# Kernel tuning notes

Measured on AMD Instinct MI355X. Metric: run time of the kernel, lower is better.

The kernel has to match this reference:

```python
import jax, jax.numpy as jnp
import numpy as np
import math

B, NH, SQ, HD = 4, 32, 512, 128
MLEN = 3584


def setup_inputs() -> dict:
    key = jax.random.key(0)
    k1, k2, k3, k4 = jax.random.split(key, 4)
    q = jax.random.normal(k1, (B, NH, SQ, HD), dtype=jnp.float32)
    k = jax.random.normal(k2, (B, NH, SQ, HD), dtype=jnp.float32)
    v = jax.random.normal(k3, (B, NH, SQ, HD), dtype=jnp.float32)
    mem = jax.random.normal(k4, (B, MLEN, 2 * NH * HD), dtype=jnp.float32)
    mask = jnp.ones((B, 1, SQ, MLEN + SQ), dtype=jnp.float32)
    return {"q": q, "k": k, "v": v, "mask": mask, "mem": mem}


def reference(q, k, v, mask, mem):
    b, nh, sq, hd = k.shape
    mlen = mem.shape[1]
    # cache_kv: stack (k,v) -> (2,b,nh,sq,hd), permute -> (b,sq,2,nh,hd), flatten
    cache_kv = jnp.stack((k, v)).transpose(1, 3, 0, 2, 4).reshape(b, sq, 2 * nh * hd)
    # split cached mem into memk/memv: (b,mlen,2,nh,hd) -> (2,b,nh,mlen,hd)
    mem_r = mem.reshape(b, mlen, 2, nh, hd).transpose(2, 0, 3, 1, 4)
    k_full = jnp.concatenate([mem_r[0], k], axis=2)  # [b,nh,mlen+sq,hd]
    v_full = jnp.concatenate([mem_r[1], v], axis=2)
    scale = 1.0 / math.sqrt(hd)
    scores = jnp.einsum("bhqd,bhkd->bhqk", q * scale, k_full)
    # standard_attention general mask path (mask.shape[-2] != 1)
    scores = scores * mask - 10000.0 * (1.0 - mask)
    probs = jax.nn.softmax(scores, axis=-1)
    context = jnp.einsum("bhqk,bhkd->bhqd", probs, v_full)
    return context, cache_kv
```

## Files before the change

kernel.cpp:

```cpp
#include <hip/hip_runtime.h>

#define B_ 4
#define NH_ 32
#define SQ_ 512
#define HD_ 128
#define MLEN_ 3584
#define KT_ 4096
#define QB_ 128
#define KB_ 64
#define NTILE_ 64
#define MEMTILES_ 56

typedef float f32x4 __attribute__((ext_vector_type(4)));
typedef short s16x8 __attribute__((ext_vector_type(8)));

__device__ __forceinline__ f32x4 MFMA16(s16x8 a, s16x8 b, f32x4 c) {
    return __builtin_amdgcn_mfma_f32_16x16x32_bf16(a, b, c, 0, 0, 0);
}

__device__ __forceinline__ s16x8 cvt8(float4 a, float4 b) {
    union { s16x8 v; __bf16 h[8]; } u;
    u.h[0] = (__bf16)a.x; u.h[1] = (__bf16)a.y;
    u.h[2] = (__bf16)a.z; u.h[3] = (__bf16)a.w;
    u.h[4] = (__bf16)b.x; u.h[5] = (__bf16)b.y;
    u.h[6] = (__bf16)b.z; u.h[7] = (__bf16)b.w;
    return u.v;
}

__launch_bounds__(512, 4)
__global__ void attn_kernel(const float* __restrict__ q, const float* __restrict__ k,
                            const float* __restrict__ v, const float* __restrict__ mask,
                            const float* __restrict__ mem, float* __restrict__ ctx)
{
    __shared__ __bf16 Klds[KB_ * HD_];
    __shared__ __bf16 Vt[HD_ * KB_];

    const int tid  = threadIdx.x;
    const int lane = tid & 63;
    const int w    = tid >> 6;
    const int l15  = lane & 15;
    const int l4   = lane >> 4;
    const int xv   = (lane & 7) << 4;

    const int qt   = blockIdx.x >> 7;
    const int pair = blockIdx.x & 127;
    const int b    = pair >> 5;
    const int h    = pair & 31;
    const int q0   = qt * QB_;

    const float scale = 0.088388347648318447f;
    s16x8 qf[4];
    {
        const float* qbase = q + (((size_t)(b * NH_ + h)) * SQ_ + q0 + w * 16 + l15) * HD_;
        #pragma unroll
        for (int kc = 0; kc < 4; ++kc) {
            const float* p = qbase + kc * 32 + l4 * 8;
            float4 a = *(const float4*)p;
            float4 c = *(const float4*)(p + 4);
            a.x *= scale; a.y *= scale; a.z *= scale; a.w *= scale;
            c.x *= scale; c.y *= scale; c.z *= scale; c.w *= scale;
            qf[kc] = cvt8(a, c);
        }
    }

    f32x4 acc[8];
    #pragma unroll
    for (int n = 0; n < 8; ++n) acc[n] = (f32x4){0.f, 0.f, 0.f, 0.f};

    float mrun = -3.0e38f, lrun = 0.f;

    const float* maskrow = mask + ((size_t)b * SQ_ + q0 + w * 16 + l15) * KT_;

    for (int t = 0; t < NTILE_; ++t) {
        const int kv0 = t * KB_;
        const float *srcK, *srcV;
        int rstride;
        if (t < MEMTILES_) {
            const float* mrow = mem + ((size_t)b * MLEN_ + kv0) * (2 * NH_ * HD_) + h * HD_;
            srcK = mrow;
            srcV = mrow + NH_ * HD_;
            rstride = 2 * NH_ * HD_;
        } else {
            size_t off = (((size_t)b * NH_ + h) * SQ_ + (kv0 - MLEN_)) * HD_;
            srcK = k + off;
            srcV = v + off;
            rstride = HD_;
        }

        __syncthreads();

        #pragma unroll
        for (int it = 0; it < 2; ++it) {
            int idx = tid + it * 512;
            int row = idx >> 4, cg = idx & 15;
            const float* p = srcK + (size_t)row * rstride + cg * 8;
            float4 a = *(const float4*)p;
            float4 c = *(const float4*)(p + 4);
            s16x8 vv = cvt8(a, c);
            int byte = row * 256 + ((cg * 16) ^ ((row & 7) << 4));
            *(s16x8*)((char*)Klds + byte) = vv;
        }
        #pragma unroll
        for (int it = 0; it < 2; ++it) {
            int idx = tid + it * 512;
            int hd = idx & 127, kvb = idx >> 7;
            const float* p = srcV + (size_t)(kvb * 8) * rstride + hd;
            union { s16x8 v; __bf16 hh[8]; } u;
            #pragma unroll
            for (int j = 0; j < 8; ++j) u.hh[j] = (__bf16)p[(size_t)j * rstride];
            int byte = hd * 128 + ((kvb * 16) ^ ((hd & 7) << 4));
            *(s16x8*)((char*)Vt + byte) = u.v;
        }

        __syncthreads();

        f32x4 mk[4];
        #pragma unroll
        for (int mt = 0; mt < 4; ++mt)
            mk[mt] = *(const f32x4*)(maskrow + kv0 + mt * 16 + l4 * 4);

        f32x4 st[4];
        #pragma unroll
        for (int mt = 0; mt < 4; ++mt) st[mt] = (f32x4){0.f, 0.f, 0.f, 0.f};
        #pragma unroll
        for (int mt = 0; mt < 4; ++mt) {
            #pragma unroll
            for (int kc = 0; kc < 4; ++kc) {
                s16x8 kf = *(const s16x8*)((const char*)Klds +
                            (mt * 16 + l15) * 256 + (((kc * 4 + l4) * 16) ^ xv));
                st[mt] = MFMA16(kf, qf[kc], st[mt]);
            }
        }

        #pragma unroll
        for (int mt = 0; mt < 4; ++mt)
            #pragma unroll
            for (int r = 0; r < 4; ++r)
                st[mt][r] = fmaf(mk[mt][r], st[mt][r] + 10000.f, -10000.f);

        float x0 = fmaxf(fmaxf(st[0][0], st[0][1]), fmaxf(st[0][2], st[0][3]));
        float x1 = fmaxf(fmaxf(st[1][0], st[1][1]), fmaxf(st[1][2], st[1][3]));
        float x2 = fmaxf(fmaxf(st[2][0], st[2][1]), fmaxf(st[2][2], st[2][3]));
        float x3 = fmaxf(fmaxf(st[3][0], st[3][1]), fmaxf(st[3][2], st[3][3]));
        float rm = fmaxf(fmaxf(x0, x1), fmaxf(x2, x3));
        rm = fmaxf(rm, __shfl_xor(rm, 16));
        rm = fmaxf(rm, __shfl_xor(rm, 32));

        if (!__all(rm <= mrun + 8.f)) {
            float nm = fmaxf(mrun, rm);
            float al = __expf(mrun - nm);
            mrun = nm;
            lrun *= al;
            float alr0 = __shfl(al, l4 * 4 + 0);
            float alr1 = __shfl(al, l4 * 4 + 1);
            float alr2 = __shfl(al, l4 * 4 + 2);
            float alr3 = __shfl(al, l4 * 4 + 3);
            #pragma unroll
            for (int nn = 0; nn < 8; ++nn) {
                acc[nn][0] *= alr0; acc[nn][1] *= alr1;
                acc[nn][2] *= alr2; acc[nn][3] *= alr3;
            }
        }

        float rs = 0.f;
        #pragma unroll
        for (int mt = 0; mt < 4; ++mt) {
            #pragma unroll
            for (int r = 0; r < 4; ++r) {
                float pe = __expf(st[mt][r] - mrun);
                st[mt][r] = pe;
                rs += pe;
            }
        }
        rs += __shfl_xor(rs, 16);
        rs += __shfl_xor(rs, 32);
        lrun += rs;

        union PK { int d[2]; __bf16 hh[4]; };
        PK pk0, pk1, pk2, pk3;
        pk0.hh[0]=(__bf16)st[0][0]; pk0.hh[1]=(__bf16)st[0][1]; pk0.hh[2]=(__bf16)st[0][2]; pk0.hh[3]=(__bf16)st[0][3];
        pk1.hh[0]=(__bf16)st[1][0]; pk1.hh[1]=(__bf16)st[1][1]; pk1.hh[2]=(__bf16)st[1][2]; pk1.hh[3]=(__bf16)st[1][3];
        pk2.hh[0]=(__bf16)st[2][0]; pk2.hh[1]=(__bf16)st[2][1]; pk2.hh[2]=(__bf16)st[2][2]; pk2.hh[3]=(__bf16)st[2][3];
        pk3.hh[0]=(__bf16)st[3][0]; pk3.hh[1]=(__bf16)st[3][1]; pk3.hh[2]=(__bf16)st[3][2]; pk3.hh[3]=(__bf16)st[3][3];

        const int srcA = (l4 & 1) * 32 + l15;
        const int srcB = srcA + 16;
        const int sel  = l4 >> 1;
        s16x8 pa[2];
        {
            union { int d[4]; s16x8 v; } ua;
            int a00 = __shfl(pk0.d[0], srcA), a10 = __shfl(pk1.d[0], srcA);
            int a01 = __shfl(pk0.d[1], srcA), a11 = __shfl(pk1.d[1], srcA);
            int b00 = __shfl(pk0.d[0], srcB), b10 = __shfl(pk1.d[0], srcB);
            int b01 = __shfl(pk0.d[1], srcB), b11 = __shfl(pk1.d[1], srcB);
            ua.d[0] = sel ? a10 : a00; ua.d[1] = sel ? a11 : a01;
            ua.d[2] = sel ? b10 : b00; ua.d[3] = sel ? b11 : b01;
            pa[0] = ua.v;
        }
        {
            union { int d[4]; s16x8 v; } ua;
            int a00 = __shfl(pk2.d[0], srcA), a10 = __shfl(pk3.d[0], srcA);
            int a01 = __shfl(pk2.d[1], srcA), a11 = __shfl(pk3.d[1], srcA);
            int b00 = __shfl(pk2.d[0], srcB), b10 = __shfl(pk3.d[0], srcB);
            int b01 = __shfl(pk2.d[1], srcB), b11 = __shfl(pk3.d[1], srcB);
            ua.d[0] = sel ? a10 : a00; ua.d[1] = sel ? a11 : a01;
            ua.d[2] = sel ? b10 : b00; ua.d[3] = sel ? b11 : b01;
            pa[1] = ua.v;
        }

        #pragma unroll
        for (int nn = 0; nn < 8; ++nn) {
            s16x8 vf0 = *(const s16x8*)((const char*)Vt +
                          (nn * 16 + l15) * 128 + ((l4 * 16) ^ xv));
            s16x8 vf1 = *(const s16x8*)((const char*)Vt +
                          (nn * 16 + l15) * 128 + ((64 + l4 * 16) ^ xv));
            acc[nn] = MFMA16(pa[0], vf0, acc[nn]);
            acc[nn] = MFMA16(pa[1], vf1, acc[nn]);
        }
    }

    float lr0 = __shfl(lrun, l4 * 4 + 0);
    float lr1 = __shfl(lrun, l4 * 4 + 1);
    float lr2 = __shfl(lrun, l4 * 4 + 2);
    float lr3 = __shfl(lrun, l4 * 4 + 3);
    float inv0 = 1.f / lr0, inv1 = 1.f / lr1, inv2 = 1.f / lr2, inv3 = 1.f / lr3;
    float* obase = ctx + (((size_t)(b * NH_ + h)) * SQ_ + q0 + w * 16 + l4 * 4) * HD_ + l15;
    #pragma unroll
    for (int nn = 0; nn < 8; ++nn) {
        obase[(size_t)0 * HD_ + nn * 16] = acc[nn][0] * inv0;
        obase[(size_t)1 * HD_ + nn * 16] = acc[nn][1] * inv1;
        obase[(size_t)2 * HD_ + nn * 16] = acc[nn][2] * inv2;
        obase[(size_t)3 * HD_ + nn * 16] = acc[nn][3] * inv3;
    }
}

__global__ void cachekv_kernel(const float* __restrict__ k, const float* __restrict__ v,
                               float* __restrict__ out)
{
    size_t i = ((size_t)blockIdx.x * 256 + threadIdx.x) * 4;
    unsigned f = (unsigned)i;
    unsigned d    = f & 127;
    unsigned hh   = (f >> 7) & 31;
    unsigned part = (f >> 12) & 1;
    unsigned s    = (f >> 13) & 511;
    unsigned bb   = f >> 22;
    const float* src = (part ? v : k) + (((size_t)(bb * 32u + hh)) * 512u + s) * 128u + d;
    *(float4*)(out + i) = *(const float4*)src;
}

extern "C" void kernel_launch(void* const* d_in, const int* in_sizes, int n_in,
                              void* d_out, int out_size, void* d_ws, size_t ws_size,
                              hipStream_t stream) {
    const float* q    = (const float*)d_in[0];
    const float* k    = (const float*)d_in[1];
    const float* v    = (const float*)d_in[2];
    const float* mask = (const float*)d_in[3];
    const float* mem  = (const float*)d_in[4];
    float* out = (float*)d_out;

    attn_kernel<<<dim3(B_ * NH_ * (SQ_ / QB_)), dim3(512), 0, stream>>>(q, k, v, mask, mem, out);

    const int ctx_elems = B_ * NH_ * SQ_ * HD_;
    const int ckv_elems = B_ * SQ_ * 2 * NH_ * HD_;
    cachekv_kernel<<<dim3(ckv_elems / 4 / 256), dim3(256), 0, stream>>>(k, v, out + ctx_elems);
    (void)in_sizes; (void)n_in; (void)out_size; (void)d_ws; (void)ws_size;
}
```

Baseline: 322.1 us.

## Split attention KV range in two blocks and merge partials with reduce kernel

Splits the 64 KV tiles into two halves handled by separate blocks, doubling the grid from 512 to 1024 blocks. Each block writes its unnormalized partial output plus its running max and sum, and a new reduce kernel merges the two halves with log-sum-exp rescaling. The partial outputs are staged in the cache_kv output region before that region is overwritten, and max/sum pairs go to the workspace. The aim is better occupancy across the CUs. The cost is an extra write and read of the partial outputs, one more kernel launch, and the Q load and setup being repeated per half.

```diff
diff --git a/kernel.cpp b/kernel.cpp
--- a/kernel.cpp
+++ b/kernel.cpp
@@ -10,6 +10,7 @@
 #define KB_ 64
 #define NTILE_ 64
 #define MEMTILES_ 56
+#define HTILES_ 32
 
 typedef float f32x4 __attribute__((ext_vector_type(4)));
 typedef short s16x8 __attribute__((ext_vector_type(8)));
@@ -27,10 +28,11 @@
     return u.v;
 }
 
-__launch_bounds__(512, 4)
-__global__ void attn_kernel(const float* __restrict__ q, const float* __restrict__ k,
-                            const float* __restrict__ v, const float* __restrict__ mask,
-                            const float* __restrict__ mem, float* __restrict__ ctx)
+__launch_bounds__(512)
+__global__ void attn_split_kernel(const float* __restrict__ q, const float* __restrict__ k,
+                                  const float* __restrict__ v, const float* __restrict__ mask,
+                                  const float* __restrict__ mem,
+                                  float* __restrict__ opart, float2* __restrict__ ml)
 {
     __shared__ __bf16 Klds[KB_ * HD_];
     __shared__ __bf16 Vt[HD_ * KB_];
@@ -42,11 +44,13 @@
     const int l4   = lane >> 4;
     const int xv   = (lane & 7) << 4;
 
-    const int qt   = blockIdx.x >> 7;
+    const int half = blockIdx.x >> 9;
+    const int qt   = (blockIdx.x >> 7) & 3;
     const int pair = blockIdx.x & 127;
     const int b    = pair >> 5;
     const int h    = pair & 31;
     const int q0   = qt * QB_;
+    const int t0   = half * HTILES_;
 
     const float scale = 0.088388347648318447f;
     s16x8 qf[4];
@@ -71,7 +75,7 @@
 
     const float* maskrow = mask + ((size_t)b * SQ_ + q0 + w * 16 + l15) * KT_;
 
-    for (int t = 0; t < NTILE_; ++t) {
+    for (int t = t0; t < t0 + HTILES_; ++t) {
         const int kv0 = t * KB_;
         const float *srcK, *srcV;
         int rstride;
@@ -219,19 +223,41 @@
         }
     }
 
-    float lr0 = __shfl(lrun, l4 * 4 + 0);
-    float lr1 = __shfl(lrun, l4 * 4 + 1);
-    float lr2 = __shfl(lrun, l4 * 4 + 2);
-    float lr3 = __shfl(lrun, l4 * 4 + 3);
-    float inv0 = 1.f / lr0, inv1 = 1.f / lr1, inv2 = 1.f / lr2, inv3 = 1.f / lr3;
-    float* obase = ctx + (((size_t)(b * NH_ + h)) * SQ_ + q0 + w * 16 + l4 * 4) * HD_ + l15;
+    float* obase = opart + (size_t)half * (B_ * NH_ * SQ_ * HD_) +
+                   (((size_t)(b * NH_ + h)) * SQ_ + q0 + w * 16 + l4 * 4) * HD_ + l15;
     #pragma unroll
     for (int nn = 0; nn < 8; ++nn) {
-        obase[(size_t)0 * HD_ + nn * 16] = acc[nn][0] * inv0;
-        obase[(size_t)1 * HD_ + nn * 16] = acc[nn][1] * inv1;
-        obase[(size_t)2 * HD_ + nn * 16] = acc[nn][2] * inv2;
-        obase[(size_t)3 * HD_ + nn * 16] = acc[nn][3] * inv3;
+        obase[(size_t)0 * HD_ + nn * 16] = acc[nn][0];
+        obase[(size_t)1 * HD_ + nn * 16] = acc[nn][1];
+        obase[(size_t)2 * HD_ + nn * 16] = acc[nn][2];
+        obase[(size_t)3 * HD_ + nn * 16] = acc[nn][3];
     }
+    if (l4 == 0) {
+        int row = (b * NH_ + h) * SQ_ + q0 + w * 16 + l15;
+        ml[half * (B_ * NH_ * SQ_) + row] = make_float2(mrun, lrun);
+    }
+}
+
+__global__ void reduce_kernel(const float* __restrict__ part, const float2* __restrict__ ml,
+                              float* __restrict__ ctx)
+{
+    int idx = blockIdx.x * 256 + threadIdx.x;
+    int row = idx >> 5;
+    int c4  = (idx & 31) * 4;
+    float2 a = ml[row];
+    float2 c = ml[(B_ * NH_ * SQ_) + row];
+    float mm = fmaxf(a.x, c.x);
+    float e0 = __expf(a.x - mm), e1 = __expf(c.x - mm);
+    float inv = 1.f / (a.y * e0 + c.y * e1);
+    const float4 o0 = *(const float4*)(part + (size_t)row * HD_ + c4);
+    const float4 o1 = *(const float4*)(part + (size_t)(B_ * NH_ * SQ_) * HD_ +
+                                       (size_t)row * HD_ + c4);
+    float4 o;
+    o.x = (o0.x * e0 + o1.x * e1) * inv;
+    o.y = (o0.y * e0 + o1.y * e1) * inv;
+    o.z = (o0.z * e0 + o1.z * e1) * inv;
+    o.w = (o0.w * e0 + o1.w * e1) * inv;
+    *(float4*)(ctx + (size_t)row * HD_ + c4) = o;
 }
 
 __global__ void cachekv_kernel(const float* __restrict__ k, const float* __restrict__ v,
@@ -258,10 +284,18 @@
     const float* mem  = (const float*)d_in[4];
     float* out = (float*)d_out;
 
-    attn_kernel<<<dim3(B_ * NH_ * (SQ_ / QB_)), dim3(512), 0, stream>>>(q, k, v, mask, mem, out);
-
     const int ctx_elems = B_ * NH_ * SQ_ * HD_;
     const int ckv_elems = B_ * SQ_ * 2 * NH_ * HD_;
+
+    float*  part = out + ctx_elems;
+    float2* ml   = (float2*)d_ws;
+
+    attn_split_kernel<<<dim3(2 * B_ * NH_ * (SQ_ / QB_)), dim3(512), 0, stream>>>(
+        q, k, v, mask, mem, part, ml);
+
+    reduce_kernel<<<dim3(ctx_elems / 4 / 256), dim3(256), 0, stream>>>(part, ml, out);
+
     cachekv_kernel<<<dim3(ckv_elems / 4 / 256), dim3(256), 0, stream>>>(k, v, out + ctx_elems);
-    (void)in_sizes; (void)n_in; (void)out_size; (void)d_ws; (void)ws_size;
-}
+
+    (void)in_sizes; (void)n_in; (void)out_size; (void)ws_size;
+}
```

Result: slower. 342.6 us (+6.4%).
